# Performance work log

Hardware: AMD Instinct MI355X
Metric: run time of the kernel (lower is better)

## Reference

```python
import jax, jax.numpy as jnp
import numpy as np

N, E = 65536, 524288
IN_DIM, HID_DIM, OUT_DIM = 1024, 512, 256


def setup_inputs() -> dict:
    key = jax.random.key(0)
    k1, k2, k3, k4, k5, k6 = jax.random.split(key, 6)
    h = jax.random.normal(k1, (N, IN_DIM), dtype=jnp.float32)
    src = jax.random.randint(k2, (E,), 0, N, dtype=jnp.int64)
    dst = jax.random.randint(k3, (E,), 0, N, dtype=jnp.int64)
    # Glorot-uniform weights as in DGL GraphConv
    lim1 = float(np.sqrt(6.0 / (IN_DIM + HID_DIM)))
    lim2 = float(np.sqrt(6.0 / (HID_DIM + OUT_DIM)))
    W1 = jax.random.uniform(k4, (IN_DIM, HID_DIM), jnp.float32, -lim1, lim1)
    W2 = jax.random.uniform(k5, (HID_DIM, OUT_DIM), jnp.float32, -lim2, lim2)
    b1 = jnp.zeros((HID_DIM,), jnp.float32)
    b2 = jnp.zeros((OUT_DIM,), jnp.float32)
    return {"h": h, "W1": W1, "b1": b1, "W2": W2, "b2": b2, "src": src, "dst": dst}


def _graph_conv(x, W, b, src, dst, inv_sqrt_dout, inv_sqrt_din):
    # DGL GraphConv, norm='both': D_in^{-1/2} A D_out^{-1/2} X W + b
    # Apply dense transform first (in_dim >= out_dim path in DGL) -- same math.
    x = x * inv_sqrt_dout[:, None]
    x = x @ W  # [N, out]
    agg = jax.ops.segment_sum(x[src], dst, num_segments=x.shape[0])  # scatter-add over edges
    return agg * inv_sqrt_din[:, None] + b


def reference(h, W1, b1, W2, b2, src, dst):
    n = h.shape[0]
    ones = jnp.ones((src.shape[0],), h.dtype)
    deg_out = jnp.maximum(jax.ops.segment_sum(ones, src, num_segments=n), 1.0)
    deg_in = jnp.maximum(jax.ops.segment_sum(ones, dst, num_segments=n), 1.0)
    inv_sqrt_dout = jax.lax.rsqrt(deg_out)
    inv_sqrt_din = jax.lax.rsqrt(deg_in)
    x = _graph_conv(h, W1, b1, src, dst, inv_sqrt_dout, inv_sqrt_din)
    x = jax.nn.elu(x)  # act; dropout p=0 -> identity
    out = _graph_conv(x, W2, b2, src, dst, inv_sqrt_dout, inv_sqrt_din)
    return out  # last_act = Identity
```

## Files before the change

### kernel.cpp

```cpp
#include <hip/hip_runtime.h>
#include <hip/hip_bf16.h>

#define IN_DIM 1024
#define HID 512
#define OUTD 256

typedef __attribute__((ext_vector_type(8))) short short8;
typedef __attribute__((ext_vector_type(4))) float f32x4;
typedef __attribute__((ext_vector_type(8))) unsigned short ushort8e;
typedef __attribute__((ext_vector_type(4))) unsigned short ushort4e;

template<int F> struct VecSel;
template<> struct VecSel<8> { using T = ushort8e; };
template<> struct VecSel<4> { using T = ushort4e; };


__device__ inline unsigned short f2bf(float f) {
    union { float f; unsigned u; } v; v.f = f;
    unsigned r = (v.u + 0x7FFF + ((v.u >> 16) & 1)) >> 16;
    return (unsigned short)r;
}

__device__ inline float bf2f(unsigned short u) {
    union { unsigned u; float f; } v; v.u = ((unsigned)u) << 16; return v.f;
}

__device__ inline void gload16(const void* g, void* l) {
    __builtin_amdgcn_global_load_lds(
        (const __attribute__((address_space(1))) void*)g,
        (__attribute__((address_space(3))) void*)l, 16, 0, 0);
}


__global__ void deg_kernel(const int* __restrict__ src, const int* __restrict__ dst,
                           int* __restrict__ dego, int* __restrict__ degi, int E) {
    int i = blockIdx.x * blockDim.x + threadIdx.x;
    if (i < E) {
        atomicAdd(&dego[src[i]], 1);
        atomicAdd(&degi[dst[i]], 1);
    }
}

__global__ void invsqrt_kernel(const int* __restrict__ dego, const int* __restrict__ degi,
                               float* __restrict__ iso, float* __restrict__ isi, int n) {
    int i = blockIdx.x * blockDim.x + threadIdx.x;
    if (i < n) {
        iso[i] = rsqrtf(fmaxf((float)dego[i], 1.0f));
        isi[i] = rsqrtf(fmaxf((float)degi[i], 1.0f));
    }
}


__global__ __launch_bounds__(256) void scan_block(const int* __restrict__ deg,
                                                  int* __restrict__ excl,
                                                  int* __restrict__ partials) {
    __shared__ int tmp[256];
    int tid = threadIdx.x;
    int i = blockIdx.x * 256 + tid;
    int v = deg[i];
    tmp[tid] = v;
    __syncthreads();
    #pragma unroll
    for (int off = 1; off < 256; off <<= 1) {
        int t = (tid >= off) ? tmp[tid - off] : 0;
        __syncthreads();
        tmp[tid] += t;
        __syncthreads();
    }
    excl[i] = tmp[tid] - v;
    if (tid == 255) partials[blockIdx.x] = tmp[255];
}

__global__ __launch_bounds__(256) void scan_partials(int* __restrict__ partials) {
    __shared__ int tmp[256];
    int tid = threadIdx.x;
    int v = partials[tid];
    tmp[tid] = v;
    __syncthreads();
    #pragma unroll
    for (int off = 1; off < 256; off <<= 1) {
        int t = (tid >= off) ? tmp[tid - off] : 0;
        __syncthreads();
        tmp[tid] += t;
        __syncthreads();
    }
    partials[tid] = tmp[tid] - v;
}

__global__ __launch_bounds__(256) void scan_add(const int* __restrict__ excl,
                                                const int* __restrict__ partials,
                                                const int* __restrict__ deg,
                                                int* __restrict__ row_start,
                                                int* __restrict__ cursor, int n) {
    int i = blockIdx.x * 256 + threadIdx.x;
    int v = excl[i] + partials[blockIdx.x];
    row_start[i] = v;
    cursor[i] = v;
    if (i == n - 1) row_start[n] = v + deg[i];
}

__global__ void csr_fill(const int* __restrict__ src, const int* __restrict__ dst,
                         int* __restrict__ cursor, int* __restrict__ eidx, int E) {
    int e = blockIdx.x * blockDim.x + threadIdx.x;
    if (e < E) {
        int pos = atomicAdd(&cursor[dst[e]], 1);
        eidx[pos] = src[e];
    }
}


__global__ __launch_bounds__(256) void scale_cvt(
    const float* __restrict__ x, const float* __restrict__ rs,
    unsigned short* __restrict__ y, int logK, size_t total)
{
    const size_t stride = (size_t)gridDim.x * 256 * 8;
    for (size_t i = ((size_t)blockIdx.x * 256 + threadIdx.x) * 8; i < total; i += stride) {
        float s = rs[i >> logK];
        float4 a = *reinterpret_cast<const float4*>(x + i);
        float4 b = *reinterpret_cast<const float4*>(x + i + 4);
        short8 o;
        o[0] = (short)f2bf(a.x * s); o[1] = (short)f2bf(a.y * s);
        o[2] = (short)f2bf(a.z * s); o[3] = (short)f2bf(a.w * s);
        o[4] = (short)f2bf(b.x * s); o[5] = (short)f2bf(b.y * s);
        o[6] = (short)f2bf(b.z * s); o[7] = (short)f2bf(b.w * s);
        *reinterpret_cast<short8*>(y + i) = o;
    }
}

__global__ void transpose_cvt(const float* __restrict__ W, unsigned short* __restrict__ Wt,
                              int K, int N) {
    int i = blockIdx.x * 256 + threadIdx.x;
    if (i < N * K) {
        int n = i / K, k = i - n * K;
        Wt[i] = f2bf(W[(size_t)k * N + n]);
    }
}


#define TM 128
#define TN 128
#define TK 32
#define NXCD 8

__global__ __launch_bounds__(256) void gemm_bf16_mfma(
    const unsigned short* __restrict__ A,
    const unsigned short* __restrict__ Bt,
    unsigned short* __restrict__ Cb,
    int M, int K, int Nc)
{
    __shared__ unsigned short As[TM][TK];
    __shared__ unsigned short Bs[TN][TK];

    const int tid  = threadIdx.x;
    const int lane = tid & 63;
    const int wave = tid >> 6;
    const int wr = wave >> 1, wc = wave & 1;
    const int lrow = lane & 15;
    const int lkg  = lane >> 4;

    const int nwg = gridDim.x;
    const int per = nwg / NXCD;
    const int lin = blockIdx.x;
    const int newlin = (lin % NXCD) * per + lin / NXCD;
    const int ncb = Nc / TN;
    const int m0 = (newlin / ncb) * TM;
    const int n0 = (newlin % ncb) * TN;

    const int s0 = wave * 64 + lane;
    const int s1 = s0 + 256;
    const int r0 = s0 >> 2, q0 = (s0 & 3) ^ ((s0 >> 3) & 3);
    const int r1 = s1 >> 2, q1 = (s1 & 3) ^ ((s1 >> 3) & 3);

    char* AsB = (char*)&As[0][0];
    char* BsB = (char*)&Bs[0][0];
    void* ldsA0 = AsB + wave * 1024;
    void* ldsA1 = AsB + 4096 + wave * 1024;
    void* ldsB0 = BsB + wave * 1024;
    void* ldsB1 = BsB + 4096 + wave * 1024;

    const int rslot = (lkg ^ ((lrow >> 1) & 3)) * 8;

    f32x4 acc[4][4] = {};

    const int nk = K / TK;
    for (int kt = 0; kt < nk; ++kt) {
        const int k0 = kt * TK;
        gload16(A  + (size_t)(m0 + r0) * K + k0 + q0 * 8, ldsA0);
        gload16(A  + (size_t)(m0 + r1) * K + k0 + q1 * 8, ldsA1);
        gload16(Bt + (size_t)(n0 + r0) * K + k0 + q0 * 8, ldsB0);
        gload16(Bt + (size_t)(n0 + r1) * K + k0 + q1 * 8, ldsB1);
        __syncthreads();

        short8 af[4], bfr[4];
        #pragma unroll
        for (int mi = 0; mi < 4; ++mi)
            af[mi] = *reinterpret_cast<const short8*>(&As[wr * 64 + mi * 16 + lrow][rslot]);
        #pragma unroll
        for (int ni = 0; ni < 4; ++ni)
            bfr[ni] = *reinterpret_cast<const short8*>(&Bs[wc * 64 + ni * 16 + lrow][rslot]);

        #pragma unroll
        for (int mi = 0; mi < 4; ++mi)
            #pragma unroll
            for (int ni = 0; ni < 4; ++ni)
                acc[mi][ni] = __builtin_amdgcn_mfma_f32_16x16x32_bf16(
                    af[mi], bfr[ni], acc[mi][ni], 0, 0, 0);

        __syncthreads();
    }

    #pragma unroll
    for (int mi = 0; mi < 4; ++mi)
        #pragma unroll
        for (int ni = 0; ni < 4; ++ni)
            #pragma unroll
            for (int r = 0; r < 4; ++r)
                Cb[(size_t)(m0 + wr * 64 + mi * 16 + lkg * 4 + r) * Nc
                   + (n0 + wc * 64 + ni * 16 + lrow)] = f2bf(acc[mi][ni][r]);
}


template<int DIM, bool LAYER1>
__global__ __launch_bounds__(256) void aggregate(
    const int* __restrict__ row_start, const int* __restrict__ eidx,
    const unsigned short* __restrict__ Xb, const float* __restrict__ isi,
    const float* __restrict__ iso, const float* __restrict__ bias,
    unsigned short* __restrict__ out_bf, float* __restrict__ out_f)
{
    constexpr int F = DIM / 64;
    using VecT = typename VecSel<F>::T;
    const int node = blockIdx.x * 4 + (threadIdx.x >> 6);
    const int lane = threadIdx.x & 63;

    const int beg = row_start[node];
    const int end = row_start[node + 1];
    const unsigned short* base = Xb + lane * F;

    float acc[F] = {};
    int e = beg;
    for (; e + 3 < end; e += 4) {
        int i0 = eidx[e], i1 = eidx[e + 1], i2 = eidx[e + 2], i3 = eidx[e + 3];
        VecT v0 = *reinterpret_cast<const VecT*>(base + (size_t)i0 * DIM);
        VecT v1 = *reinterpret_cast<const VecT*>(base + (size_t)i1 * DIM);
        VecT v2 = *reinterpret_cast<const VecT*>(base + (size_t)i2 * DIM);
        VecT v3 = *reinterpret_cast<const VecT*>(base + (size_t)i3 * DIM);
        #pragma unroll
        for (int f = 0; f < F; ++f) {
            acc[f] += bf2f(v0[f]); acc[f] += bf2f(v1[f]);
            acc[f] += bf2f(v2[f]); acc[f] += bf2f(v3[f]);
        }
    }
    for (; e < end; ++e) {
        VecT v0 = *reinterpret_cast<const VecT*>(base + (size_t)eidx[e] * DIM);
        #pragma unroll
        for (int f = 0; f < F; ++f) acc[f] += bf2f(v0[f]);
    }

    const float si = isi[node];
    float bv[F];
    #pragma unroll
    for (int q = 0; q < F / 4; ++q)
        *reinterpret_cast<float4*>(&bv[q * 4]) =
            *reinterpret_cast<const float4*>(bias + lane * F + q * 4);

    if (LAYER1) {
        const float so = iso[node];
        short8 o;
        #pragma unroll
        for (int f = 0; f < F; ++f) {
            float v = acc[f] * si + bv[f];
            v = v > 0.f ? v : expm1f(v);
            o[f] = (short)f2bf(v * so);
        }
        *reinterpret_cast<short8*>(out_bf + (size_t)node * DIM + lane * F) = o;
    } else {
        #pragma unroll
        for (int q = 0; q < F / 4; ++q) {
            float4 v = make_float4(acc[q * 4 + 0] * si + bv[q * 4 + 0],
                                   acc[q * 4 + 1] * si + bv[q * 4 + 1],
                                   acc[q * 4 + 2] * si + bv[q * 4 + 2],
                                   acc[q * 4 + 3] * si + bv[q * 4 + 3]);
            *reinterpret_cast<float4*>(out_f + (size_t)node * DIM + lane * F + q * 4) = v;
        }
    }
}


extern "C" void kernel_launch(void* const* d_in, const int* in_sizes, int n_in,
                              void* d_out, int out_size, void* d_ws, size_t ws_size,
                              hipStream_t stream) {
    const float* h  = (const float*)d_in[0];
    const float* W1 = (const float*)d_in[1];
    const float* b1 = (const float*)d_in[2];
    const float* W2 = (const float*)d_in[3];
    const float* b2 = (const float*)d_in[4];
    const int*   src = (const int*)d_in[5];
    const int*   dst = (const int*)d_in[6];

    const int N = in_sizes[0] / IN_DIM;
    const int E = in_sizes[5];
    float* out = (float*)d_out;

    int* dego      = (int*)d_ws;
    int* degi      = dego + N;
    int* excl      = degi + N;
    int* partials  = excl + N;
    int* row_start = partials + 256;
    int* cursor    = row_start + N + 64;
    int* eidx      = cursor + N;
    float* iso     = (float*)(eidx + E);
    float* isi     = iso + N;
    unsigned short* W1t = (unsigned short*)(isi + N);
    unsigned short* W2t = W1t + (size_t)IN_DIM * HID;
    unsigned short* hb  = W2t + (size_t)HID * OUTD;
    unsigned short* X1b = hb + (size_t)N * IN_DIM;
    unsigned short* X2b = X1b;
    unsigned short* R2h = X1b + (size_t)N * HID;

    hipMemsetAsync(dego, 0, sizeof(int) * (size_t)2 * N, stream);

    deg_kernel<<<(E + 255) / 256, 256, 0, stream>>>(src, dst, dego, degi, E);
    invsqrt_kernel<<<(N + 255) / 256, 256, 0, stream>>>(dego, degi, iso, isi, N);

    scan_block<<<N / 256, 256, 0, stream>>>(degi, excl, partials);
    scan_partials<<<1, 256, 0, stream>>>(partials);
    scan_add<<<N / 256, 256, 0, stream>>>(excl, partials, degi, row_start, cursor, N);
    csr_fill<<<(E + 255) / 256, 256, 0, stream>>>(src, dst, cursor, eidx, E);

    scale_cvt<<<2048, 256, 0, stream>>>(h, iso, hb, 10, (size_t)N * IN_DIM);
    transpose_cvt<<<(IN_DIM * HID + 255) / 256, 256, 0, stream>>>(W1, W1t, IN_DIM, HID);
    transpose_cvt<<<(HID * OUTD + 255) / 256, 256, 0, stream>>>(W2, W2t, HID, OUTD);

    gemm_bf16_mfma<<<(N / TM) * (HID / TN), 256, 0, stream>>>(
        hb, W1t, X1b, N, IN_DIM, HID);
    aggregate<HID, true><<<N / 4, 256, 0, stream>>>(
        row_start, eidx, X1b, isi, iso, b1, R2h, nullptr);

    gemm_bf16_mfma<<<(N / TM) * (OUTD / TN), 256, 0, stream>>>(
        R2h, W2t, X2b, N, HID, OUTD);
    aggregate<OUTD, false><<<N / 4, 256, 0, stream>>>(
        row_start, eidx, X2b, isi, iso, b2, nullptr, out);
}
```

Before: 443.2 us.

## Fuse fp32-to-bf16 conversion into GEMM and move source scaling into aggregation

Removes the separate scale_cvt pass over h. The first GEMM now reads fp32 h directly and converts it to bf16 in registers, and the per-source D_out^{-1/2} scaling moves into the layer-1 aggregation as an FMA per edge. Both GEMMs drop LDS staging and syncthreads and load fragments straight from global memory. This saves a full read and write of the large input, but each wave reloads A and B with no LDS sharing, so global and L2 traffic rise and the GEMM may become memory-bound. The bf16 packing also changes from round-to-nearest-even to round-half-up.

```diff
diff --git a/kernel.cpp b/kernel.cpp
--- a/kernel.cpp
+++ b/kernel.cpp
@@ -9,6 +9,7 @@
 typedef __attribute__((ext_vector_type(4))) float f32x4;
 typedef __attribute__((ext_vector_type(8))) unsigned short ushort8e;
 typedef __attribute__((ext_vector_type(4))) unsigned short ushort4e;
+typedef __attribute__((ext_vector_type(4))) unsigned int uint4e;
 
 template<int F> struct VecSel;
 template<> struct VecSel<8> { using T = ushort8e; };
@@ -25,10 +26,14 @@
     union { unsigned u; float f; } v; v.u = ((unsigned)u) << 16; return v.f;
 }
 
-__device__ inline void gload16(const void* g, void* l) {
-    __builtin_amdgcn_global_load_lds(
-        (const __attribute__((address_space(1))) void*)g,
-        (__attribute__((address_space(3))) void*)l, 16, 0, 0);
+__device__ inline unsigned pk2(float a, float b) {
+    unsigned ua = __float_as_uint(a) + 0x8000u;
+    unsigned ub = __float_as_uint(b) + 0x8000u;
+#if __has_builtin(__builtin_amdgcn_perm)
+    return __builtin_amdgcn_perm(ub, ua, 0x07060302u);
+#else
+    return (ua >> 16) | (ub & 0xFFFF0000u);
+#endif
 }
 
 
@@ -109,24 +114,6 @@
 }
 
 
-__global__ __launch_bounds__(256) void scale_cvt(
-    const float* __restrict__ x, const float* __restrict__ rs,
-    unsigned short* __restrict__ y, int logK, size_t total)
-{
-    const size_t stride = (size_t)gridDim.x * 256 * 8;
-    for (size_t i = ((size_t)blockIdx.x * 256 + threadIdx.x) * 8; i < total; i += stride) {
-        float s = rs[i >> logK];
-        float4 a = *reinterpret_cast<const float4*>(x + i);
-        float4 b = *reinterpret_cast<const float4*>(x + i + 4);
-        short8 o;
-        o[0] = (short)f2bf(a.x * s); o[1] = (short)f2bf(a.y * s);
-        o[2] = (short)f2bf(a.z * s); o[3] = (short)f2bf(a.w * s);
-        o[4] = (short)f2bf(b.x * s); o[5] = (short)f2bf(b.y * s);
-        o[6] = (short)f2bf(b.z * s); o[7] = (short)f2bf(b.w * s);
-        *reinterpret_cast<short8*>(y + i) = o;
-    }
-}
-
 __global__ void transpose_cvt(const float* __restrict__ W, unsigned short* __restrict__ Wt,
                               int K, int N) {
     int i = blockIdx.x * 256 + threadIdx.x;
@@ -139,18 +126,13 @@
 
 #define TM 128
 #define TN 128
-#define TK 32
 #define NXCD 8
 
-__global__ __launch_bounds__(256) void gemm_bf16_mfma(
-    const unsigned short* __restrict__ A,
-    const unsigned short* __restrict__ Bt,
-    unsigned short* __restrict__ Cb,
-    int M, int K, int Nc)
+template<int AF32, int KC, int NC>
+__global__ __launch_bounds__(256) void gemm_direct(
+    const void* __restrict__ Ap, const unsigned short* __restrict__ Bt,
+    unsigned short* __restrict__ Cb, int M)
 {
-    __shared__ unsigned short As[TM][TK];
-    __shared__ unsigned short Bs[TN][TK];
-
     const int tid  = threadIdx.x;
     const int lane = tid & 63;
     const int wave = tid >> 6;
@@ -162,42 +144,49 @@
     const int per = nwg / NXCD;
     const int lin = blockIdx.x;
     const int newlin = (lin % NXCD) * per + lin / NXCD;
-    const int ncb = Nc / TN;
+    const int ncb = NC / TN;
     const int m0 = (newlin / ncb) * TM;
     const int n0 = (newlin % ncb) * TN;
 
-    const int s0 = wave * 64 + lane;
-    const int s1 = s0 + 256;
-    const int r0 = s0 >> 2, q0 = (s0 & 3) ^ ((s0 >> 3) & 3);
-    const int r1 = s1 >> 2, q1 = (s1 & 3) ^ ((s1 >> 3) & 3);
-
-    char* AsB = (char*)&As[0][0];
-    char* BsB = (char*)&Bs[0][0];
-    void* ldsA0 = AsB + wave * 1024;
-    void* ldsA1 = AsB + 4096 + wave * 1024;
-    void* ldsB0 = BsB + wave * 1024;
-    void* ldsB1 = BsB + 4096 + wave * 1024;
-
-    const int rslot = (lkg ^ ((lrow >> 1) & 3)) * 8;
+    const float* Af = (const float*)Ap;
+    const unsigned short* Ab = (const unsigned short*)Ap;
+
+    const float* pAf[4];
+    const unsigned short* pAb[4];
+    const unsigned short* pB[4];
+    #pragma unroll
+    for (int mi = 0; mi < 4; ++mi) {
+        const int row = m0 + wr * 64 + mi * 16 + lrow;
+        if (AF32) pAf[mi] = Af + (size_t)row * KC + lkg * 8;
+        else      pAb[mi] = Ab + (size_t)row * KC + lkg * 8;
+    }
+    #pragma unroll
+    for (int ni = 0; ni < 4; ++ni) {
+        const int col = n0 + wc * 64 + ni * 16 + lrow;
+        pB[ni] = Bt + (size_t)col * KC + lkg * 8;
+    }
 
     f32x4 acc[4][4] = {};
 
-    const int nk = K / TK;
-    for (int kt = 0; kt < nk; ++kt) {
-        const int k0 = kt * TK;
-        gload16(A  + (size_t)(m0 + r0) * K + k0 + q0 * 8, ldsA0);
-        gload16(A  + (size_t)(m0 + r1) * K + k0 + q1 * 8, ldsA1);
-        gload16(Bt + (size_t)(n0 + r0) * K + k0 + q0 * 8, ldsB0);
-        gload16(Bt + (size_t)(n0 + r1) * K + k0 + q1 * 8, ldsB1);
-        __syncthreads();
-
+    #pragma unroll 4
+    for (int kt = 0; kt < KC / 32; ++kt) {
         short8 af[4], bfr[4];
         #pragma unroll
-        for (int mi = 0; mi < 4; ++mi)
-            af[mi] = *reinterpret_cast<const short8*>(&As[wr * 64 + mi * 16 + lrow][rslot]);
+        for (int mi = 0; mi < 4; ++mi) {
+            if (AF32) {
+                float4 x = *reinterpret_cast<const float4*>(pAf[mi] + kt * 32);
+                float4 y = *reinterpret_cast<const float4*>(pAf[mi] + kt * 32 + 4);
+                uint4e u;
+                u[0] = pk2(x.x, x.y); u[1] = pk2(x.z, x.w);
+                u[2] = pk2(y.x, y.y); u[3] = pk2(y.z, y.w);
+                af[mi] = *reinterpret_cast<short8*>(&u);
+            } else {
+                af[mi] = *reinterpret_cast<const short8*>(pAb[mi] + kt * 32);
+            }
+        }
         #pragma unroll
         for (int ni = 0; ni < 4; ++ni)
-            bfr[ni] = *reinterpret_cast<const short8*>(&Bs[wc * 64 + ni * 16 + lrow][rslot]);
+            bfr[ni] = *reinterpret_cast<const short8*>(pB[ni] + kt * 32);
 
         #pragma unroll
         for (int mi = 0; mi < 4; ++mi)
@@ -205,8 +194,6 @@
             for (int ni = 0; ni < 4; ++ni)
                 acc[mi][ni] = __builtin_amdgcn_mfma_f32_16x16x32_bf16(
                     af[mi], bfr[ni], acc[mi][ni], 0, 0, 0);
-
-        __syncthreads();
     }
 
     #pragma unroll
@@ -215,7 +202,7 @@
         for (int ni = 0; ni < 4; ++ni)
             #pragma unroll
             for (int r = 0; r < 4; ++r)
-                Cb[(size_t)(m0 + wr * 64 + mi * 16 + lkg * 4 + r) * Nc
+                Cb[(size_t)(m0 + wr * 64 + mi * 16 + lkg * 4 + r) * NC
                    + (n0 + wc * 64 + ni * 16 + lrow)] = f2bf(acc[mi][ni][r]);
 }
 
@@ -240,20 +227,32 @@
     int e = beg;
     for (; e + 3 < end; e += 4) {
         int i0 = eidx[e], i1 = eidx[e + 1], i2 = eidx[e + 2], i3 = eidx[e + 3];
+        float s0 = 1.f, s1 = 1.f, s2 = 1.f, s3 = 1.f;
+        if (LAYER1) { s0 = iso[i0]; s1 = iso[i1]; s2 = iso[i2]; s3 = iso[i3]; }
         VecT v0 = *reinterpret_cast<const VecT*>(base + (size_t)i0 * DIM);
         VecT v1 = *reinterpret_cast<const VecT*>(base + (size_t)i1 * DIM);
         VecT v2 = *reinterpret_cast<const VecT*>(base + (size_t)i2 * DIM);
         VecT v3 = *reinterpret_cast<const VecT*>(base + (size_t)i3 * DIM);
         #pragma unroll
         for (int f = 0; f < F; ++f) {
-            acc[f] += bf2f(v0[f]); acc[f] += bf2f(v1[f]);
-            acc[f] += bf2f(v2[f]); acc[f] += bf2f(v3[f]);
+            if (LAYER1) {
+                acc[f] = fmaf(s0, bf2f(v0[f]), acc[f]);
+                acc[f] = fmaf(s1, bf2f(v1[f]), acc[f]);
+                acc[f] = fmaf(s2, bf2f(v2[f]), acc[f]);
+                acc[f] = fmaf(s3, bf2f(v3[f]), acc[f]);
+            } else {
+                acc[f] += bf2f(v0[f]); acc[f] += bf2f(v1[f]);
+                acc[f] += bf2f(v2[f]); acc[f] += bf2f(v3[f]);
+            }
         }
     }
     for (; e < end; ++e) {
-        VecT v0 = *reinterpret_cast<const VecT*>(base + (size_t)eidx[e] * DIM);
-        #pragma unroll
-        for (int f = 0; f < F; ++f) acc[f] += bf2f(v0[f]);
+        int i0 = eidx[e];
+        float s0 = LAYER1 ? iso[i0] : 1.f;
+        VecT v0 = *reinterpret_cast<const VecT*>(base + (size_t)i0 * DIM);
+        #pragma unroll
+        for (int f = 0; f < F; ++f)
+            acc[f] = LAYER1 ? fmaf(s0, bf2f(v0[f]), acc[f]) : acc[f] + bf2f(v0[f]);
     }
 
     const float si = isi[node];
@@ -312,8 +311,7 @@
     float* isi     = iso + N;
     unsigned short* W1t = (unsigned short*)(isi + N);
     unsigned short* W2t = W1t + (size_t)IN_DIM * HID;
-    unsigned short* hb  = W2t + (size_t)HID * OUTD;
-    unsigned short* X1b = hb + (size_t)N * IN_DIM;
+    unsigned short* X1b = W2t + (size_t)HID * OUTD;
     unsigned short* X2b = X1b;
     unsigned short* R2h = X1b + (size_t)N * HID;
 
@@ -327,17 +325,16 @@
     scan_add<<<N / 256, 256, 0, stream>>>(excl, partials, degi, row_start, cursor, N);
     csr_fill<<<(E + 255) / 256, 256, 0, stream>>>(src, dst, cursor, eidx, E);
 
-    scale_cvt<<<2048, 256, 0, stream>>>(h, iso, hb, 10, (size_t)N * IN_DIM);
     transpose_cvt<<<(IN_DIM * HID + 255) / 256, 256, 0, stream>>>(W1, W1t, IN_DIM, HID);
     transpose_cvt<<<(HID * OUTD + 255) / 256, 256, 0, stream>>>(W2, W2t, HID, OUTD);
 
-    gemm_bf16_mfma<<<(N / TM) * (HID / TN), 256, 0, stream>>>(
-        hb, W1t, X1b, N, IN_DIM, HID);
+    gemm_direct<1, IN_DIM, HID><<<(N / TM) * (HID / TN), 256, 0, stream>>>(
+        h, W1t, X1b, N);
     aggregate<HID, true><<<N / 4, 256, 0, stream>>>(
         row_start, eidx, X1b, isi, iso, b1, R2h, nullptr);
 
-    gemm_bf16_mfma<<<(N / TM) * (OUTD / TN), 256, 0, stream>>>(
-        R2h, W2t, X2b, N, HID, OUTD);
+    gemm_direct<0, HID, OUTD><<<(N / TM) * (OUTD / TN), 256, 0, stream>>>(
+        R2h, W2t, X2b, N);
     aggregate<OUTD, false><<<N / 4, 256, 0, stream>>>(
         row_start, eidx, X2b, isi, iso, b2, nullptr, out);
 }
```

After: 648.9 us. +46.4%, slower.

## Double-buffer GEMM LDS tiles with vmcnt-based prefetch and tile the weight transpose

Applied to the files above, without the earlier changes.

Gives the bf16 MFMA GEMM two LDS buffers and prefetches the tile two steps ahead with direct global-to-LDS loads. It waits with a partial vmcnt so loads overlap the MFMA work, instead of a full load-sync-compute-sync cycle per K step. The weight transpose now runs through a padded shared-memory tile so both its reads and writes are coalesced. This doubles LDS use per block, which may lower occupancy, and relies on hand-placed waitcnt and barrier ordering being correct.

```diff
diff --git a/kernel.cpp b/kernel.cpp
--- a/kernel.cpp
+++ b/kernel.cpp
@@ -127,29 +127,37 @@
     }
 }
 
-__global__ void transpose_cvt(const float* __restrict__ W, unsigned short* __restrict__ Wt,
-                              int K, int N) {
-    int i = blockIdx.x * 256 + threadIdx.x;
-    if (i < N * K) {
-        int n = i / K, k = i - n * K;
-        Wt[i] = f2bf(W[(size_t)k * N + n]);
-    }
-}
-
-
-#define TM 128
-#define TN 128
-#define TK 32
+__global__ __launch_bounds__(256) void transpose_cvt_tiled(
+    const float* __restrict__ W, unsigned short* __restrict__ Wt, int K, int N)
+{
+    __shared__ unsigned short tile[32][33];
+    const int tx = threadIdx.x & 31;
+    const int ty = threadIdx.x >> 5;
+    const int n0 = blockIdx.x * 32;
+    const int k0 = blockIdx.y * 32;
+
+    #pragma unroll
+    for (int j = 0; j < 4; ++j) {
+        int k = ty + j * 8;
+        tile[k][tx] = f2bf(W[(size_t)(k0 + k) * N + n0 + tx]);
+    }
+    __syncthreads();
+    #pragma unroll
+    for (int j = 0; j < 4; ++j) {
+        int n = ty + j * 8;
+        Wt[(size_t)(n0 + n) * K + k0 + tx] = tile[tx][n];
+    }
+}
+
+
 #define NXCD 8
 
-__global__ __launch_bounds__(256) void gemm_bf16_mfma(
-    const unsigned short* __restrict__ A,
-    const unsigned short* __restrict__ Bt,
-    unsigned short* __restrict__ Cb,
-    int M, int K, int Nc)
+__global__ __launch_bounds__(256) void gemm_cnt(
+    const unsigned short* __restrict__ Ab, const unsigned short* __restrict__ Bt,
+    unsigned short* __restrict__ Cb, int M, int K, int Nc)
 {
-    __shared__ unsigned short As[TM][TK];
-    __shared__ unsigned short Bs[TN][TK];
+    __shared__ unsigned short As[2][128][32];
+    __shared__ unsigned short Bs[2][128][32];
 
     const int tid  = threadIdx.x;
     const int lane = tid & 63;
@@ -158,46 +166,49 @@
     const int lrow = lane & 15;
     const int lkg  = lane >> 4;
 
-    const int nwg = gridDim.x;
-    const int per = nwg / NXCD;
-    const int lin = blockIdx.x;
-    const int newlin = (lin % NXCD) * per + lin / NXCD;
-    const int ncb = Nc / TN;
-    const int m0 = (newlin / ncb) * TM;
-    const int n0 = (newlin % ncb) * TN;
+    const int per = gridDim.x / NXCD;
+    const int newlin = (blockIdx.x % NXCD) * per + blockIdx.x / NXCD;
+    const int ncb = Nc / 128;
+    const int m0 = (newlin / ncb) * 128;
+    const int n0 = (newlin % ncb) * 128;
 
     const int s0 = wave * 64 + lane;
     const int s1 = s0 + 256;
     const int r0 = s0 >> 2, q0 = (s0 & 3) ^ ((s0 >> 3) & 3);
     const int r1 = s1 >> 2, q1 = (s1 & 3) ^ ((s1 >> 3) & 3);
 
-    char* AsB = (char*)&As[0][0];
-    char* BsB = (char*)&Bs[0][0];
-    void* ldsA0 = AsB + wave * 1024;
-    void* ldsA1 = AsB + 4096 + wave * 1024;
-    void* ldsB0 = BsB + wave * 1024;
-    void* ldsB1 = BsB + 4096 + wave * 1024;
+    char* AsB = (char*)&As[0][0][0];
+    char* BsB = (char*)&Bs[0][0][0];
+
+    auto stage = [&](int kt, int buf) {
+        const int k0 = kt * 32;
+        gload16(Ab + (size_t)(m0 + r0) * K + k0 + q0 * 8, AsB + buf * 8192 + wave * 1024);
+        gload16(Ab + (size_t)(m0 + r1) * K + k0 + q1 * 8, AsB + buf * 8192 + 4096 + wave * 1024);
+        gload16(Bt + (size_t)(n0 + r0) * K + k0 + q0 * 8, BsB + buf * 8192 + wave * 1024);
+        gload16(Bt + (size_t)(n0 + r1) * K + k0 + q1 * 8, BsB + buf * 8192 + 4096 + wave * 1024);
+    };
 
     const int rslot = (lkg ^ ((lrow >> 1) & 3)) * 8;
 
     f32x4 acc[4][4] = {};
 
-    const int nk = K / TK;
+    stage(0, 0);
+    stage(1, 1);
+    asm volatile("s_waitcnt vmcnt(4)" ::: "memory");
+    __builtin_amdgcn_sched_barrier(0);
+    __builtin_amdgcn_s_barrier();
+
+    const int nk = K / 32;
     for (int kt = 0; kt < nk; ++kt) {
-        const int k0 = kt * TK;
-        gload16(A  + (size_t)(m0 + r0) * K + k0 + q0 * 8, ldsA0);
-        gload16(A  + (size_t)(m0 + r1) * K + k0 + q1 * 8, ldsA1);
-        gload16(Bt + (size_t)(n0 + r0) * K + k0 + q0 * 8, ldsB0);
-        gload16(Bt + (size_t)(n0 + r1) * K + k0 + q1 * 8, ldsB1);
-        __syncthreads();
+        const int cur = kt & 1;
 
         short8 af[4], bfr[4];
         #pragma unroll
         for (int mi = 0; mi < 4; ++mi)
-            af[mi] = *reinterpret_cast<const short8*>(&As[wr * 64 + mi * 16 + lrow][rslot]);
+            af[mi] = *reinterpret_cast<const short8*>(&As[cur][wr * 64 + mi * 16 + lrow][rslot]);
         #pragma unroll
         for (int ni = 0; ni < 4; ++ni)
-            bfr[ni] = *reinterpret_cast<const short8*>(&Bs[wc * 64 + ni * 16 + lrow][rslot]);
+            bfr[ni] = *reinterpret_cast<const short8*>(&Bs[cur][wc * 64 + ni * 16 + lrow][rslot]);
 
         #pragma unroll
         for (int mi = 0; mi < 4; ++mi)
@@ -206,7 +217,16 @@
                 acc[mi][ni] = __builtin_amdgcn_mfma_f32_16x16x32_bf16(
                     af[mi], bfr[ni], acc[mi][ni], 0, 0, 0);
 
-        __syncthreads();
+        __builtin_amdgcn_s_barrier();
+
+        if (kt + 2 < nk) {
+            stage(kt + 2, cur);
+            asm volatile("s_waitcnt vmcnt(4)" ::: "memory");
+        } else {
+            asm volatile("s_waitcnt vmcnt(0)" ::: "memory");
+        }
+        __builtin_amdgcn_sched_barrier(0);
+        __builtin_amdgcn_s_barrier();
     }
 
     #pragma unroll
@@ -328,15 +348,19 @@
     csr_fill<<<(E + 255) / 256, 256, 0, stream>>>(src, dst, cursor, eidx, E);
 
     scale_cvt<<<2048, 256, 0, stream>>>(h, iso, hb, 10, (size_t)N * IN_DIM);
-    transpose_cvt<<<(IN_DIM * HID + 255) / 256, 256, 0, stream>>>(W1, W1t, IN_DIM, HID);
-    transpose_cvt<<<(HID * OUTD + 255) / 256, 256, 0, stream>>>(W2, W2t, HID, OUTD);
-
-    gemm_bf16_mfma<<<(N / TM) * (HID / TN), 256, 0, stream>>>(
+    {
+        dim3 g1(HID / 32, IN_DIM / 32);
+        transpose_cvt_tiled<<<g1, 256, 0, stream>>>(W1, W1t, IN_DIM, HID);
+        dim3 g2(OUTD / 32, HID / 32);
+        transpose_cvt_tiled<<<g2, 256, 0, stream>>>(W2, W2t, HID, OUTD);
+    }
+
+    gemm_cnt<<<(N / 128) * (HID / 128), 256, 0, stream>>>(
         hb, W1t, X1b, N, IN_DIM, HID);
     aggregate<HID, true><<<N / 4, 256, 0, stream>>>(
         row_start, eidx, X1b, isi, iso, b1, R2h, nullptr);
 
-    gemm_bf16_mfma<<<(N / TM) * (OUTD / TN), 256, 0, stream>>>(
+    gemm_cnt<<<(N / 128) * (OUTD / 128), 256, 0, stream>>>(
         R2h, W2t, X2b, N, HID, OUTD);
     aggregate<OUTD, false><<<N / 4, 256, 0, stream>>>(
         row_start, eidx, X2b, isi, iso, b2, nullptr, out);
```

Result: no change. 445.0 us (+0.4%).
